# Kernel optimization log

Measured on AMD Instinct MI355X. Metric: run time of the kernel, lower is better.

The kernel has to match this reference:

```python
import jax, jax.numpy as jnp
import numpy as np

B, T, D = 128, 512, 400
N_VALS, N_ACTS = 1024, 128

def setup_inputs() -> dict:
    key = jax.random.key(0)
    ks = jax.random.split(key, 7)
    H_utt = jax.random.normal(ks[0], (B, T, D), dtype=jnp.float32)
    c_utt = jax.random.normal(ks[1], (B, D), dtype=jnp.float32)
    C_acts = jax.random.normal(ks[2], (B, N_ACTS, D), dtype=jnp.float32)
    C_vals = jax.random.normal(ks[3], (N_VALS, 1, D), dtype=jnp.float32)
    W_score = jax.random.normal(ks[4], (1, D), dtype=jnp.float32) * (1.0 / np.sqrt(D))
    b_score = jnp.zeros((1,), dtype=jnp.float32)
    lens = jax.random.randint(ks[5], (B,), T // 2, T + 1, dtype=jnp.int64 if jax.config.read('jax_enable_x64') else jnp.int32)
    lens = lens.at[0].set(T)  # ensure max(lens) == T so masking matches torch semantics
    return {"H_utt": H_utt, "c_utt": c_utt, "C_acts": C_acts, "C_vals": C_vals,
            "W_score": W_score, "b_score": b_score, "utterance_len": lens}

def reference(H_utt, c_utt, C_acts, C_vals, W_score, b_score, utterance_len):
    vals = C_vals[:, 0, :]                                   # [V, D]
    # --- y_utts: default attention of each value vector over utterance states ---
    scores = jnp.einsum('btd,vd->bvt', H_utt, vals)          # mul+sum scoring
    mask = jnp.arange(T)[None, :] < utterance_len[:, None]   # [B, T]
    scores = jnp.where(mask[:, None, :], scores, -jnp.inf)
    probs = jax.nn.softmax(scores, axis=-1)                  # [B, V, T]
    q_utts = jnp.einsum('bvt,btd->bvd', probs, H_utt)        # weighted sum contexts
    y_utts = jnp.einsum('bvd,d->bv', q_utts, W_score[0]) + b_score[0]  # utt_scorer
    # --- y_acts: attention of c_utt over per-example act vectors, then score vs vals ---
    s2 = jnp.einsum('bad,bd->ba', C_acts, c_utt)
    p2 = jax.nn.softmax(s2, axis=-1)
    q_acts = jnp.einsum('ba,bad->bd', p2, C_acts)            # [B, D]
    y_acts = q_acts @ vals.T                                 # [B, V]
    return (y_utts, y_acts)
```

## Files before the change

kernel.cpp:

```cpp
#include <hip/hip_runtime.h>
#include <hip/hip_bf16.h>

#define B_  128
#define T_  512
#define D_  400
#define NV  1024
#define NA  128

#define LDH  416
#define NT   32
#define MV   64
#define LOG2E 1.4426950408889634f

typedef __bf16 bf16_t;
typedef bf16_t bf16x8 __attribute__((ext_vector_type(8)));
typedef float  floatx4 __attribute__((ext_vector_type(4)));

__device__ inline void async_copy16(const void* g, void* l) {
    __builtin_amdgcn_global_load_lds(
        (const __attribute__((address_space(1))) unsigned int*)g,
        (__attribute__((address_space(3))) unsigned int*)l, 16, 0, 0);
}

__device__ inline float dot4(float4 a, float4 b) {
    return a.x * b.x + a.y * b.y + a.z * b.z + a.w * b.w;
}

template<int PRE>
__global__ __launch_bounds__(256) void prep_kernel(const float* __restrict__ H,
                                                   const float* __restrict__ W,
                                                   const float* __restrict__ cu,
                                                   const float* __restrict__ Ca,
                                                   float* __restrict__ hw,
                                                   bf16_t* __restrict__ Hbf,
                                                   float* __restrict__ q_ws) {
    __shared__ __align__(16) float4 cu4[100];
    __shared__ float s_lds[NA];
    __shared__ float p_lds[NA];
    __shared__ float red[8];
    __shared__ __align__(16) float4 part[100];

    int tid = threadIdx.x, wave = tid >> 6, lane = tid & 63;

    if (blockIdx.x >= 128) {
        long wid = (long)(blockIdx.x - 128) * 4 + wave;
        long r0 = wid * 8;
        const float* base = H + r0 * D_;
        float acc[8];
#pragma unroll
        for (int j = 0; j < 8; ++j) acc[j] = 0.f;

        if (lane < 50) {
            float4 wx = ((const float4*)W)[lane * 2];
            float4 wy = ((const float4*)W)[lane * 2 + 1];
            bf16_t* ob = Hbf + r0 * (long)LDH;
            int pos = lane;
#pragma unroll
            for (int j = 0; j < 8; ++j) {
                const float4* p = (const float4*)(base + (long)j * D_ + lane * 8);
                float4 x = p[0], y = p[1];
                acc[j] = dot4(x, wx) + dot4(y, wy);
                if (PRE) {
                    bf16x8 f;
                    f[0] = (bf16_t)x.x; f[1] = (bf16_t)x.y;
                    f[2] = (bf16_t)x.z; f[3] = (bf16_t)x.w;
                    f[4] = (bf16_t)y.x; f[5] = (bf16_t)y.y;
                    f[6] = (bf16_t)y.z; f[7] = (bf16_t)y.w;
                    int pj = (lane < 48) ? (pos ^ j) : pos;
                    *(bf16x8*)(ob + (long)j * LDH + pj * 8) = f;
                }
            }
        } else if (PRE && lane < 52) {
            bf16x8 z;
#pragma unroll
            for (int jj = 0; jj < 8; ++jj) z[jj] = (bf16_t)0.0f;
            bf16_t* ob = Hbf + r0 * (long)LDH + lane * 8;
#pragma unroll
            for (int j = 0; j < 8; ++j)
                *(bf16x8*)(ob + (long)j * LDH) = z;
        }

#pragma unroll
        for (int off = 1; off < 64; off <<= 1) {
#pragma unroll
            for (int j = 0; j < 8; ++j) acc[j] += __shfl_xor(acc[j], off, 64);
        }
        if (lane == 0) {
#pragma unroll
            for (int j = 0; j < 8; ++j) hw[r0 + j] = acc[j];
        }
        return;
    }

    int b = blockIdx.x;

    if (tid < 100) cu4[tid] = ((const float4*)(cu + (size_t)b * D_))[tid];
    __syncthreads();

    const float4* Cb4 = (const float4*)(Ca + (size_t)b * NA * D_);
#pragma unroll 2
    for (int i = 0; i < 32; ++i) {
        int a = wave * 32 + i;
        const float4* row = Cb4 + (size_t)a * 100;
        float acc = dot4(row[lane], cu4[lane]);
        if (lane < 36) acc += dot4(row[lane + 64], cu4[lane + 64]);
#pragma unroll
        for (int off = 1; off < 64; off <<= 1) acc += __shfl_xor(acc, off, 64);
        if (lane == 0) s_lds[a] = acc;
    }
    __syncthreads();

    float s = (tid < NA) ? s_lds[tid] : -3.0e38f;
    float m = s;
#pragma unroll
    for (int off = 1; off < 64; off <<= 1) m = fmaxf(m, __shfl_xor(m, off, 64));
    if (lane == 0) red[wave] = m;
    __syncthreads();
    m = fmaxf(red[0], red[1]);
    float e = (tid < NA) ? __expf(s - m) : 0.f;
    float sum = e;
#pragma unroll
    for (int off = 1; off < 64; off <<= 1) sum += __shfl_xor(sum, off, 64);
    if (lane == 0) red[4 + wave] = sum;
    __syncthreads();
    float S = red[4] + red[5];
    if (tid < NA) p_lds[tid] = e / S;
    __syncthreads();

    int c4 = tid % 100;
    int half = tid / 100;
    float4 acc0 = {0.f, 0.f, 0.f, 0.f};
    if (tid < 200) {
        float4 acc1 = {0.f, 0.f, 0.f, 0.f};
        int a0 = half * 64;
#pragma unroll 4
        for (int a = 0; a < 64; a += 2) {
            float p0 = p_lds[a0 + a], p1 = p_lds[a0 + a + 1];
            float4 x0 = Cb4[(size_t)(a0 + a) * 100 + c4];
            float4 x1 = Cb4[(size_t)(a0 + a + 1) * 100 + c4];
            acc0.x += p0 * x0.x; acc0.y += p0 * x0.y; acc0.z += p0 * x0.z; acc0.w += p0 * x0.w;
            acc1.x += p1 * x1.x; acc1.y += p1 * x1.y; acc1.z += p1 * x1.z; acc1.w += p1 * x1.w;
        }
        acc0.x += acc1.x; acc0.y += acc1.y; acc0.z += acc1.z; acc0.w += acc1.w;
        if (half == 1) part[c4] = acc0;
    }
    __syncthreads();
    if (tid < 100) {
        float4 o = part[c4];
        o.x += acc0.x; o.y += acc0.y; o.z += acc0.z; o.w += acc0.w;
        ((float4*)(q_ws + (size_t)b * D_))[c4] = o;
    }
}

template<int PRE>
__global__ __launch_bounds__(256, 3) void main_kernel(const float* __restrict__ H,
                                                      const bf16_t* __restrict__ Hbf,
                                                      const float* __restrict__ Cv,
                                                      const float* __restrict__ hw,
                                                      const float* __restrict__ q_ws,
                                                      const float* __restrict__ bs,
                                                      const int* __restrict__ lens,
                                                      float* __restrict__ out) {
    __shared__ bf16_t h_lds[2][NT * LDH];

    int i = blockIdx.x;
    int xcd = i & 7, vc = (i >> 3) & 15, bb = i >> 7;
    int b = xcd + 8 * bb;
    int vbase = vc * MV;

    int tid = threadIdx.x;
    int wave = tid >> 6, lane = tid & 63;
    int lrow = lane & 15, quad = lane >> 4;

    int len = lens[b];
    float b0 = bs[0];

    if (!PRE) {
        for (int idx = tid; idx < 2 * NT * 2; idx += 256) {
            int bu = idx >> 6, rem = idx & 63;
            int r = rem >> 1, c = 50 + (rem & 1);
            bf16x8 z;
#pragma unroll
            for (int j = 0; j < 8; ++j) z[j] = (bf16_t)0.0f;
            *(bf16x8*)((char*)h_lds[bu] + r * 832 + c * 16) = z;
        }
    }

    bf16x8 afrag[13];
    {
        const float* vrow = Cv + (size_t)(vbase + wave * 16 + lrow) * D_;
#pragma unroll
        for (int kk = 0; kk < 13; ++kk) {
            int k0 = kk * 32 + quad * 8;
            bf16x8 f;
            if (k0 >= D_) {
#pragma unroll
                for (int j = 0; j < 8; ++j) f[j] = (bf16_t)0.0f;
            } else {
                const float4* p = (const float4*)(vrow + k0);
                float4 x = p[0], y = p[1];
                f[0] = (bf16_t)(x.x * LOG2E); f[1] = (bf16_t)(x.y * LOG2E);
                f[2] = (bf16_t)(x.z * LOG2E); f[3] = (bf16_t)(x.w * LOG2E);
                f[4] = (bf16_t)(y.x * LOG2E); f[5] = (bf16_t)(y.y * LOG2E);
                f[6] = (bf16_t)(y.z * LOG2E); f[7] = (bf16_t)(y.w * LOG2E);
            }
            afrag[kk] = f;
        }
    }

    float m_s[4], l_s[4], a_s[4];
#pragma unroll
    for (int r = 0; r < 4; ++r) { m_s[r] = -3.0e38f; l_s[r] = 0.f; a_s[r] = 0.f; }

    int ntiles = (len + NT - 1) / NT;
    const float* Hb = H + (size_t)b * T_ * D_;
    const bf16_t* Hbfb = Hbf + (size_t)b * T_ * LDH;
    const float* hwb = hw + (size_t)b * T_;

    auto stage = [&](int buf, int tt) {
        if (PRE) {
            const char* gt = (const char*)(Hbfb + (size_t)tt * NT * LDH);
            char* lt = (char*)h_lds[buf];
#pragma unroll 1
            for (int off = tid * 16; off < NT * LDH * 2; off += 4096)
                async_copy16(gt + off, lt + off);
        } else {
            for (int idx = tid; idx < NT * 50; idx += 256) {
                int r = idx / 50, c = idx - r * 50;
                const float4* s = (const float4*)(Hb + (size_t)(tt * NT + r) * D_ + c * 8);
                float4 x = s[0], y = s[1];
                bf16x8 f;
                f[0] = (bf16_t)x.x; f[1] = (bf16_t)x.y; f[2] = (bf16_t)x.z; f[3] = (bf16_t)x.w;
                f[4] = (bf16_t)y.x; f[5] = (bf16_t)y.y; f[6] = (bf16_t)y.z; f[7] = (bf16_t)y.w;
                int pos = (c < 48) ? (c ^ (r & 7)) : c;
                *(bf16x8*)((char*)h_lds[buf] + r * 832 + pos * 16) = f;
            }
        }
    };

    stage(0, 0);
    __syncthreads();

    const int swz = (lrow & 7) << 4;
    const int rowb0 = lrow * 832;
    const int rowb1 = (16 + lrow) * 832;

    for (int tt = 0; tt < ntiles; ++tt) {
        int cur = tt & 1;
        if (tt + 1 < ntiles) stage(cur ^ 1, tt + 1);

        int t0 = tt * NT;
        float hwv[2];
#pragma unroll
        for (int s = 0; s < 2; ++s) hwv[s] = hwb[t0 + s * 16 + lrow];

        floatx4 c0 = {0.f, 0.f, 0.f, 0.f};
        floatx4 c1 = {0.f, 0.f, 0.f, 0.f};

        const char* L = (const char*)h_lds[cur];
#pragma unroll
        for (int kk = 0; kk < 13; ++kk) {
            int koffb = kk * 64 + quad * 16;
            int o = (kk < 12) ? (koffb ^ swz) : koffb;
            bf16x8 f0 = *(const bf16x8*)(L + rowb0 + o);
            c0 = __builtin_amdgcn_mfma_f32_16x16x32_bf16(afrag[kk], f0, c0, 0, 0, 0);
            bf16x8 f1 = *(const bf16x8*)(L + rowb1 + o);
            c1 = __builtin_amdgcn_mfma_f32_16x16x32_bf16(afrag[kk], f1, c1, 0, 0, 0);
        }

        if (t0 + NT > len) {
            if (t0 + lrow >= len) {
                c0[0] = -3.0e38f; c0[1] = -3.0e38f; c0[2] = -3.0e38f; c0[3] = -3.0e38f;
            }
            if (t0 + 16 + lrow >= len) {
                c1[0] = -3.0e38f; c1[1] = -3.0e38f; c1[2] = -3.0e38f; c1[3] = -3.0e38f;
            }
        }

#pragma unroll
        for (int r = 0; r < 4; ++r) {
            float cm = fmaxf(c0[r], c1[r]);
            float mn = fmaxf(m_s[r], cm);
            float alpha = __builtin_amdgcn_exp2f(m_s[r] - mn);
            float p0 = __builtin_amdgcn_exp2f(c0[r] - mn);
            float p1 = __builtin_amdgcn_exp2f(c1[r] - mn);
            l_s[r] = l_s[r] * alpha + p0 + p1;
            a_s[r] = a_s[r] * alpha + p0 * hwv[0] + p1 * hwv[1];
            m_s[r] = mn;
        }

        __syncthreads();
    }

#pragma unroll
    for (int r = 0; r < 4; ++r) {
        float m = m_s[r], l = l_s[r], a = a_s[r];
#pragma unroll
        for (int off = 1; off < 16; off <<= 1) {
            float mo = __shfl_xor(m, off, 64);
            float lo = __shfl_xor(l, off, 64);
            float ao = __shfl_xor(a, off, 64);
            float mn = fmaxf(m, mo);
            float f1 = __builtin_amdgcn_exp2f(m - mn);
            float f2 = __builtin_amdgcn_exp2f(mo - mn);
            l = l * f1 + lo * f2;
            a = a * f1 + ao * f2;
            m = mn;
        }
        if (lrow == 0) {
            int v = vbase + wave * 16 + quad * 4 + r;
            out[(size_t)b * NV + v] = a / l + b0;
        }
    }

    {
        const float4* q4 = (const float4*)(q_ws + (size_t)b * D_);
        float4 qa = q4[lane];
        float4 qb = (lane < 36) ? q4[lane + 64] : make_float4(0.f, 0.f, 0.f, 0.f);
#pragma unroll 1
        for (int ii = 0; ii < 16; ii += 4) {
            int v0 = vbase + wave * 16 + ii;
            float acc[4];
#pragma unroll
            for (int r = 0; r < 4; ++r) {
                const float4* v4 = (const float4*)(Cv + (size_t)(v0 + r) * D_);
                acc[r] = dot4(v4[lane], qa);
                if (lane < 36) acc[r] += dot4(v4[lane + 64], qb);
            }
#pragma unroll
            for (int off = 1; off < 64; off <<= 1) {
#pragma unroll
                for (int r = 0; r < 4; ++r) acc[r] += __shfl_xor(acc[r], off, 64);
            }
            if (lane == 0) {
                float4 o = make_float4(acc[0], acc[1], acc[2], acc[3]);
                *(float4*)(out + (size_t)B_ * NV + (size_t)b * NV + v0) = o;
            }
        }
    }
}

extern "C" void kernel_launch(void* const* d_in, const int* in_sizes, int n_in,
                              void* d_out, int out_size, void* d_ws, size_t ws_size,
                              hipStream_t stream) {
    const float* H    = (const float*)d_in[0];
    const float* cu   = (const float*)d_in[1];
    const float* Ca   = (const float*)d_in[2];
    const float* Cv   = (const float*)d_in[3];
    const float* W    = (const float*)d_in[4];
    const float* bs   = (const float*)d_in[5];
    const int*   lens = (const int*)d_in[6];
    float* out = (float*)d_out;

    float*  hw   = (float*)d_ws;
    float*  q_ws = hw + (size_t)B_ * T_;
    bf16_t* Hbf  = (bf16_t*)(q_ws + (size_t)B_ * D_);

    size_t need = ((size_t)B_ * T_ + (size_t)B_ * D_) * sizeof(float)
                + (size_t)B_ * T_ * LDH * sizeof(bf16_t);
    bool pre = (ws_size >= need);

    dim3 pgrid(128 + 2048);
    if (pre) {
        prep_kernel<1><<<pgrid, dim3(256), 0, stream>>>(H, W, cu, Ca, hw, Hbf, q_ws);
        main_kernel<1><<<dim3(2048), dim3(256), 0, stream>>>(H, Hbf, Cv, hw, q_ws, bs, lens, out);
    } else {
        prep_kernel<0><<<pgrid, dim3(256), 0, stream>>>(H, W, cu, Ca, hw, Hbf, q_ws);
        main_kernel<0><<<dim3(2048), dim3(256), 0, stream>>>(H, Hbf, Cv, hw, q_ws, bs, lens, out);
    }
}
```

Measured before the change: 308.5 us.

## Interleave async tile prefetch with MFMA phases and add lazy softmax rescaling

Splits the next tile's async global-to-LDS copy into three chunks that are issued between three MFMA phases, separated by raw s_barrier calls and raised wave priority around the MFMA blocks. The single __syncthreads is replaced by an explicit vmcnt wait plus barrier. The online softmax now skips the rescale when no row max grows by more than a threshold across the wave, which cuts exp2 and multiply work. The intent is to overlap memory traffic with matrix compute and trim ALU work in the softmax, at the cost of more barriers and a more complex synchronisation scheme.

```diff
diff --git a/kernel.cpp b/kernel.cpp
--- a/kernel.cpp
+++ b/kernel.cpp
@@ -54,7 +54,6 @@
             float4 wx = ((const float4*)W)[lane * 2];
             float4 wy = ((const float4*)W)[lane * 2 + 1];
             bf16_t* ob = Hbf + r0 * (long)LDH;
-            int pos = lane;
 #pragma unroll
             for (int j = 0; j < 8; ++j) {
                 const float4* p = (const float4*)(base + (long)j * D_ + lane * 8);
@@ -66,7 +65,7 @@
                     f[2] = (bf16_t)x.z; f[3] = (bf16_t)x.w;
                     f[4] = (bf16_t)y.x; f[5] = (bf16_t)y.y;
                     f[6] = (bf16_t)y.z; f[7] = (bf16_t)y.w;
-                    int pj = (lane < 48) ? (pos ^ j) : pos;
+                    int pj = (lane < 48) ? (lane ^ j) : lane;
                     *(bf16x8*)(ob + (long)j * LDH + pj * 8) = f;
                 }
             }
@@ -217,29 +216,39 @@
     const bf16_t* Hbfb = Hbf + (size_t)b * T_ * LDH;
     const float* hwb = hw + (size_t)b * T_;
 
-    auto stage = [&](int buf, int tt) {
-        if (PRE) {
-            const char* gt = (const char*)(Hbfb + (size_t)tt * NT * LDH);
-            char* lt = (char*)h_lds[buf];
-#pragma unroll 1
-            for (int off = tid * 16; off < NT * LDH * 2; off += 4096)
-                async_copy16(gt + off, lt + off);
-        } else {
-            for (int idx = tid; idx < NT * 50; idx += 256) {
-                int r = idx / 50, c = idx - r * 50;
-                const float4* s = (const float4*)(Hb + (size_t)(tt * NT + r) * D_ + c * 8);
-                float4 x = s[0], y = s[1];
-                bf16x8 f;
-                f[0] = (bf16_t)x.x; f[1] = (bf16_t)x.y; f[2] = (bf16_t)x.z; f[3] = (bf16_t)x.w;
-                f[4] = (bf16_t)y.x; f[5] = (bf16_t)y.y; f[6] = (bf16_t)y.z; f[7] = (bf16_t)y.w;
-                int pos = (c < 48) ? (c ^ (r & 7)) : c;
-                *(bf16x8*)((char*)h_lds[buf] + r * 832 + pos * 16) = f;
-            }
+    auto stage_part = [&](int buf, int tt, int k0, int k1) {
+        const char* gt = (const char*)(Hbfb + (size_t)tt * NT * LDH);
+        char* lt = (char*)h_lds[buf];
+        int cbase = wave * 416 + lane;
+#pragma unroll
+        for (int k = k0; k < k1; ++k) {
+            int c = cbase + (k << 6);
+            if (lane + (k << 6) < 416)
+                async_copy16(gt + c * 16, lt + c * 16);
         }
     };
 
-    stage(0, 0);
-    __syncthreads();
+    auto stage_f32 = [&](int buf, int tt) {
+        for (int idx = tid; idx < NT * 50; idx += 256) {
+            int r = idx / 50, c = idx - r * 50;
+            const float4* s = (const float4*)(Hb + (size_t)(tt * NT + r) * D_ + c * 8);
+            float4 x = s[0], y = s[1];
+            bf16x8 f;
+            f[0] = (bf16_t)x.x; f[1] = (bf16_t)x.y; f[2] = (bf16_t)x.z; f[3] = (bf16_t)x.w;
+            f[4] = (bf16_t)y.x; f[5] = (bf16_t)y.y; f[6] = (bf16_t)y.z; f[7] = (bf16_t)y.w;
+            int pos = (c < 48) ? (c ^ (r & 7)) : c;
+            *(bf16x8*)((char*)h_lds[buf] + r * 832 + pos * 16) = f;
+        }
+    };
+
+    if (PRE) {
+        stage_part(0, 0, 0, 7);
+        asm volatile("s_waitcnt vmcnt(0)" ::: "memory");
+        __builtin_amdgcn_s_barrier();
+    } else {
+        stage_f32(0, 0);
+        __syncthreads();
+    }
 
     const int swz = (lrow & 7) << 4;
     const int rowb0 = lrow * 832;
@@ -247,26 +256,66 @@
 
     for (int tt = 0; tt < ntiles; ++tt) {
         int cur = tt & 1;
-        if (tt + 1 < ntiles) stage(cur ^ 1, tt + 1);
-
-        int t0 = tt * NT;
-        float hwv[2];
-#pragma unroll
-        for (int s = 0; s < 2; ++s) hwv[s] = hwb[t0 + s * 16 + lrow];
+        bool pre_next = (tt + 1 < ntiles);
+        const char* L = (const char*)h_lds[cur];
 
         floatx4 c0 = {0.f, 0.f, 0.f, 0.f};
         floatx4 c1 = {0.f, 0.f, 0.f, 0.f};
 
-        const char* L = (const char*)h_lds[cur];
-#pragma unroll
-        for (int kk = 0; kk < 13; ++kk) {
-            int koffb = kk * 64 + quad * 16;
-            int o = (kk < 12) ? (koffb ^ swz) : koffb;
-            bf16x8 f0 = *(const bf16x8*)(L + rowb0 + o);
-            c0 = __builtin_amdgcn_mfma_f32_16x16x32_bf16(afrag[kk], f0, c0, 0, 0, 0);
-            bf16x8 f1 = *(const bf16x8*)(L + rowb1 + o);
-            c1 = __builtin_amdgcn_mfma_f32_16x16x32_bf16(afrag[kk], f1, c1, 0, 0, 0);
-        }
+        if (PRE) {
+            if (pre_next) stage_part(cur ^ 1, tt + 1, 0, 3);
+            __builtin_amdgcn_s_setprio(1);
+#pragma unroll
+            for (int kk = 0; kk < 4; ++kk) {
+                int o = (kk * 64 + quad * 16) ^ swz;
+                bf16x8 f0 = *(const bf16x8*)(L + rowb0 + o);
+                c0 = __builtin_amdgcn_mfma_f32_16x16x32_bf16(afrag[kk], f0, c0, 0, 0, 0);
+                bf16x8 f1 = *(const bf16x8*)(L + rowb1 + o);
+                c1 = __builtin_amdgcn_mfma_f32_16x16x32_bf16(afrag[kk], f1, c1, 0, 0, 0);
+            }
+            __builtin_amdgcn_s_setprio(0);
+            __builtin_amdgcn_s_barrier();
+
+            if (pre_next) stage_part(cur ^ 1, tt + 1, 3, 5);
+            __builtin_amdgcn_s_setprio(1);
+#pragma unroll
+            for (int kk = 4; kk < 8; ++kk) {
+                int o = (kk * 64 + quad * 16) ^ swz;
+                bf16x8 f0 = *(const bf16x8*)(L + rowb0 + o);
+                c0 = __builtin_amdgcn_mfma_f32_16x16x32_bf16(afrag[kk], f0, c0, 0, 0, 0);
+                bf16x8 f1 = *(const bf16x8*)(L + rowb1 + o);
+                c1 = __builtin_amdgcn_mfma_f32_16x16x32_bf16(afrag[kk], f1, c1, 0, 0, 0);
+            }
+            __builtin_amdgcn_s_setprio(0);
+            __builtin_amdgcn_s_barrier();
+
+            if (pre_next) stage_part(cur ^ 1, tt + 1, 5, 7);
+            __builtin_amdgcn_s_setprio(1);
+#pragma unroll
+            for (int kk = 8; kk < 13; ++kk) {
+                int koffb = kk * 64 + quad * 16;
+                int o = (kk < 12) ? (koffb ^ swz) : koffb;
+                bf16x8 f0 = *(const bf16x8*)(L + rowb0 + o);
+                c0 = __builtin_amdgcn_mfma_f32_16x16x32_bf16(afrag[kk], f0, c0, 0, 0, 0);
+                bf16x8 f1 = *(const bf16x8*)(L + rowb1 + o);
+                c1 = __builtin_amdgcn_mfma_f32_16x16x32_bf16(afrag[kk], f1, c1, 0, 0, 0);
+            }
+            __builtin_amdgcn_s_setprio(0);
+        } else {
+#pragma unroll
+            for (int kk = 0; kk < 13; ++kk) {
+                int koffb = kk * 64 + quad * 16;
+                int o = (kk < 12) ? (koffb ^ swz) : koffb;
+                bf16x8 f0 = *(const bf16x8*)(L + rowb0 + o);
+                c0 = __builtin_amdgcn_mfma_f32_16x16x32_bf16(afrag[kk], f0, c0, 0, 0, 0);
+                bf16x8 f1 = *(const bf16x8*)(L + rowb1 + o);
+                c1 = __builtin_amdgcn_mfma_f32_16x16x32_bf16(afrag[kk], f1, c1, 0, 0, 0);
+            }
+        }
+
+        int t0 = tt * NT;
+        float hwv0 = hwb[t0 + lrow];
+        float hwv1 = hwb[t0 + 16 + lrow];
 
         if (t0 + NT > len) {
             if (t0 + lrow >= len) {
@@ -277,19 +326,42 @@
             }
         }
 
+        float cm[4];
+        bool grow = false;
 #pragma unroll
         for (int r = 0; r < 4; ++r) {
-            float cm = fmaxf(c0[r], c1[r]);
-            float mn = fmaxf(m_s[r], cm);
-            float alpha = __builtin_amdgcn_exp2f(m_s[r] - mn);
-            float p0 = __builtin_amdgcn_exp2f(c0[r] - mn);
-            float p1 = __builtin_amdgcn_exp2f(c1[r] - mn);
-            l_s[r] = l_s[r] * alpha + p0 + p1;
-            a_s[r] = a_s[r] * alpha + p0 * hwv[0] + p1 * hwv[1];
-            m_s[r] = mn;
-        }
-
-        __syncthreads();
+            cm[r] = fmaxf(c0[r], c1[r]);
+            grow = grow || (cm[r] > m_s[r] + 8.0f);
+        }
+        if (__builtin_amdgcn_ballot_w64(grow) != 0ull) {
+#pragma unroll
+            for (int r = 0; r < 4; ++r) {
+                float mn = fmaxf(m_s[r], cm[r]);
+                float alpha = __builtin_amdgcn_exp2f(m_s[r] - mn);
+                float p0 = __builtin_amdgcn_exp2f(c0[r] - mn);
+                float p1 = __builtin_amdgcn_exp2f(c1[r] - mn);
+                l_s[r] = l_s[r] * alpha + p0 + p1;
+                a_s[r] = a_s[r] * alpha + p0 * hwv0 + p1 * hwv1;
+                m_s[r] = mn;
+            }
+        } else {
+#pragma unroll
+            for (int r = 0; r < 4; ++r) {
+                float p0 = __builtin_amdgcn_exp2f(c0[r] - m_s[r]);
+                float p1 = __builtin_amdgcn_exp2f(c1[r] - m_s[r]);
+                l_s[r] = l_s[r] + p0 + p1;
+                a_s[r] = a_s[r] + p0 * hwv0 + p1 * hwv1;
+            }
+        }
+
+        if (PRE) {
+            asm volatile("s_waitcnt vmcnt(0)" ::: "memory");
+            __builtin_amdgcn_s_barrier();
+        } else {
+            __syncthreads();
+            if (pre_next) stage_f32(cur ^ 1, tt + 1);
+            __syncthreads();
+        }
     }
 
 #pragma unroll
```

After: 312.2 us. Within noise of the previous version (+1.2%).
